# Kernel optimization log

Measured on AMD Instinct MI355X. Metric: run time of the kernel, lower is better.

Reference implementation:

```python
import jax, jax.numpy as jnp
import numpy as np

N_NODES = 100000
N_EDGES = 1600000
N_GRAPHS = 1024
F_NODE = 16
F_EDGE = 8
F_GRAPH = 10
F_OUT = 1
H = 64
EPS = 1e-7  # GENConv eps
T = 1.0     # GENConv softmax temperature (learn_t=False default)


def _lin_init(key, fi, fo):
    kw, kb = jax.random.split(key)
    s = 1.0 / np.sqrt(fi)
    W = jax.random.uniform(kw, (fi, fo), jnp.float32, -s, s)
    b = jax.random.uniform(kb, (fo,), jnp.float32, -s, s)
    return W, b


def setup_inputs() -> dict:
    key = jax.random.key(0)
    ks = jax.random.split(key, 24)
    inp = {
        'x': jax.random.normal(ks[0], (N_NODES, F_NODE), jnp.float32),
        'edge_attr': jax.random.normal(ks[1], (N_EDGES, F_EDGE), jnp.float32),
        'graph_attr': jax.random.normal(ks[2], (N_GRAPHS, F_GRAPH), jnp.float32),
        'edge_index': jax.random.randint(ks[3], (2, N_EDGES), 0, N_NODES),
        'batch': jnp.sort(jax.random.randint(ks[4], (N_NODES,), 0, N_GRAPHS)),
    }
    inp['node_W'], inp['node_b'] = _lin_init(ks[5], F_NODE, H)
    inp['edge_W'], inp['edge_b'] = _lin_init(ks[6], F_EDGE, H)
    # three GENConv MLPs: Linear(H,2H) -> BN(identity @eval) -> ReLU -> Linear(2H,H)
    for i, k1, k2 in ((1, ks[7], ks[8]), (2, ks[9], ks[10]), (3, ks[11], ks[12])):
        inp[f'c{i}_W1'], inp[f'c{i}_b1'] = _lin_init(k1, H, 2 * H)
        inp[f'c{i}_W2'], inp[f'c{i}_b2'] = _lin_init(k2, 2 * H, H)
    inp['d1_W'], inp['d1_b'] = _lin_init(ks[13], H + F_GRAPH, 32)
    inp['d2_W'], inp['d2_b'] = _lin_init(ks[14], 32, 32)
    inp['out_W'], inp['out_b'] = _lin_init(ks[15], 32, F_OUT)
    return inp


def _genconv(h, src, dst, ea, W1, b1, W2, b2):
    # message: relu(x_j + edge_attr) + eps   [E, H]
    msg = jax.nn.relu(h[src] + ea) + EPS
    # per-destination, per-feature segment softmax (aggr='softmax', t=1)
    m = jax.ops.segment_max(msg * T, dst, num_segments=N_NODES)   # [N, H]
    e = jnp.exp(msg * T - m[dst])                                  # [E, H]
    denom = jax.ops.segment_sum(e, dst, num_segments=N_NODES)     # [N, H]
    alpha = e / jnp.maximum(denom[dst], 1e-16)
    agg = jax.ops.segment_sum(msg * alpha, dst, num_segments=N_NODES)
    out = h + agg  # root add
    # MLP (BatchNorm is identity in eval with default stats)
    hid = jax.nn.relu(out @ W1 + b1)
    return hid @ W2 + b2


def reference(x, edge_attr, graph_attr, node_W, node_b, edge_W, edge_b,
              c1_W1, c1_b1, c1_W2, c1_b2,
              c2_W1, c2_b1, c2_W2, c2_b2,
              c3_W1, c3_b1, c3_W2, c3_b2,
              d1_W, d1_b, d2_W, d2_b, out_W, out_b,
              edge_index, batch):
    src, dst = edge_index[0], edge_index[1]
    h = x @ node_W + node_b
    ea = edge_attr @ edge_W + edge_b
    h = jax.nn.relu(_genconv(h, src, dst, ea, c1_W1, c1_b1, c1_W2, c1_b2))
    h = jax.nn.relu(_genconv(h, src, dst, ea, c2_W1, c2_b1, c2_W2, c2_b2))
    h = jax.nn.relu(_genconv(h, src, dst, ea, c3_W1, c3_b1, c3_W2, c3_b2))
    # global mean pool over graphs
    sums = jax.ops.segment_sum(h, batch, num_segments=N_GRAPHS)          # [G, H]
    cnt = jax.ops.segment_sum(jnp.ones((h.shape[0],), h.dtype), batch, num_segments=N_GRAPHS)
    pooled = sums / jnp.maximum(cnt, 1.0)[:, None]
    g = jnp.concatenate([pooled, graph_attr], axis=1)                    # [G, H+F_GRAPH]
    g = jax.nn.relu(g @ d1_W + d1_b)   # dropout = identity at eval
    g = jax.nn.relu(g @ d2_W + d2_b)
    return jax.nn.sigmoid(g @ out_W + out_b)                             # [G, 1]
```

## Files before the change

kernel.cpp:

```cpp
#include <hip/hip_runtime.h>
#include <hip/hip_bf16.h>

#define N_NODES 100000
#define N_EDGES 1600000
#define N_GRAPHS 1024
#define F_NODE 16
#define F_EDGE 8
#define F_GRAPH 10
#define HD 64
#define HD2 128
#define GEN_EPS 1e-7f
#define SCAN_NBLK ((N_NODES + 255) / 256)

typedef unsigned short u16;
typedef unsigned int u32;
typedef __attribute__((ext_vector_type(8))) short short8;
typedef __attribute__((ext_vector_type(4))) float floatx4;

__device__ __forceinline__ u16 f2bf(float x) {
    u32 u = __float_as_uint(x);
    return (u16)((u + 0x7FFFu + ((u >> 16) & 1u)) >> 16);
}
__device__ __forceinline__ float bf2f(u16 u) {
    return __uint_as_float(((u32)u) << 16);
}
__device__ __forceinline__ float u2f(unsigned int u) {
    return __uint_as_float(u);
}

__global__ void __launch_bounds__(256) k_node_embed(
        const float* __restrict__ x, const float* __restrict__ W,
        const float* __restrict__ b, float* __restrict__ h,
        u16* __restrict__ hb) {
    __shared__ float sW[F_NODE * HD];
    __shared__ float sb[HD];
    for (int i = threadIdx.x; i < F_NODE * HD; i += 256) sW[i] = W[i];
    if (threadIdx.x < HD) sb[threadIdx.x] = b[threadIdx.x];
    __syncthreads();
    int t = blockIdx.x * 256 + threadIdx.x;
    if (t >= N_NODES * HD) return;
    int n = t >> 6, f = t & 63;
    const float* xr = x + (size_t)n * F_NODE;
    float acc = sb[f];
#pragma unroll
    for (int k = 0; k < F_NODE; k++) acc += xr[k] * sW[k * HD + f];
    h[t] = acc;
    hb[t] = f2bf(acc);
}

__global__ void __launch_bounds__(256) k_hist(
        const int* __restrict__ dst, int* __restrict__ deg,
        int* __restrict__ rank) {
    int e = blockIdx.x * 256 + threadIdx.x;
    if (e >= N_EDGES) return;
    rank[e] = atomicAdd(&deg[dst[e]], 1);
}

__global__ void __launch_bounds__(256) k_scan1(
        const int* __restrict__ deg, int* __restrict__ bsum) {
    __shared__ int red[256];
    int t = threadIdx.x;
    int g = blockIdx.x * 256 + t;
    red[t] = (g < N_NODES) ? deg[g] : 0;
    __syncthreads();
    for (int s = 128; s > 0; s >>= 1) {
        if (t < s) red[t] += red[t + s];
        __syncthreads();
    }
    if (t == 0) bsum[blockIdx.x] = red[0];
}

__global__ void __launch_bounds__(512) k_scan2(
        const int* __restrict__ bsum, int* __restrict__ bpre) {
    __shared__ int sh[512];
    int t = threadIdx.x;
    int v = (t < SCAN_NBLK) ? bsum[t] : 0;
    sh[t] = v;
    __syncthreads();
    for (int d = 1; d < 512; d <<= 1) {
        int u = (t >= d) ? sh[t - d] : 0;
        __syncthreads();
        sh[t] += u;
        __syncthreads();
    }
    if (t < SCAN_NBLK) bpre[t] = sh[t] - v;
}

__global__ void __launch_bounds__(256) k_scan3(
        const int* __restrict__ deg, const int* __restrict__ bpre,
        int* __restrict__ off) {
    __shared__ int sh[256];
    int t = threadIdx.x;
    int g = blockIdx.x * 256 + t;
    int v = (g < N_NODES) ? deg[g] : 0;
    sh[t] = v;
    __syncthreads();
    for (int d = 1; d < 256; d <<= 1) {
        int u = (t >= d) ? sh[t - d] : 0;
        __syncthreads();
        sh[t] += u;
        __syncthreads();
    }
    int incl = sh[t];
    int base = bpre[blockIdx.x];
    if (g < N_NODES) off[g] = base + incl - v;
    if (g == N_NODES - 1) off[N_NODES] = base + incl;
}

__global__ void __launch_bounds__(256) k_scatter(
        const int* __restrict__ src, const int* __restrict__ dst,
        const int* __restrict__ rank, const int* __restrict__ off,
        const float* __restrict__ eattr,
        unsigned int* __restrict__ rec, int* __restrict__ srcs) {
    int e = blockIdx.x * 256 + threadIdx.x;
    if (e >= N_EDGES) return;
    const uint4* ap = reinterpret_cast<const uint4*>(eattr + (size_t)e * F_EDGE);
    uint4 a0 = ap[0], a1 = ap[1];
    int pos = off[dst[e]] + rank[e];
    uint4* op = reinterpret_cast<uint4*>(rec + (size_t)pos * 8);
    op[0] = a0;
    op[1] = a1;
    srcs[pos] = src[e];
}

__global__ void __launch_bounds__(256) k_gen_agg(
        const float* __restrict__ h, const u16* __restrict__ hb,
        const int* __restrict__ off,
        const unsigned int* __restrict__ rec,
        const int* __restrict__ srcs,
        const float* __restrict__ eW, const float* __restrict__ eb,
        float* __restrict__ outb) {
    __shared__ float sAttr[4][64];
    int wid = threadIdx.x >> 6;
    int lane = threadIdx.x & 63;
    int f = lane;
    float w[F_EDGE];
#pragma unroll
    for (int k = 0; k < F_EDGE; k++) w[k] = eW[k * HD + f];
    float bf = eb[f];
    int wave0 = blockIdx.x * 4 + wid;
    const int NW = gridDim.x * 4;
    for (int n0 = wave0; n0 < N_NODES; n0 += NW) {
        int n = __builtin_amdgcn_readfirstlane(n0);
        int beg = off[n], end = off[n + 1];
        size_t idx = (size_t)n * HD + f;
        float hroot = h[idx];
        float den = 0.f, nm = 0.f;
        if (beg < end) {
            int i = beg;
            float av = 0.f;
            if (beg + (lane >> 3) < end) av = u2f(rec[(size_t)beg * 8 + lane]);
            int s8[8];
#pragma unroll
            for (int u = 0; u < 8; u++) s8[u] = srcs[beg + u];
            while (true) {
                float hv[8];
#pragma unroll
                for (int u = 0; u < 8; u++)
                    hv[u] = bf2f(hb[(size_t)s8[u] * HD + f]);
                int inx = i + 8;
                bool more = inx < end;
                float avN = 0.f;
                int s8N[8];
                if (more) {
                    if (inx + (lane >> 3) < end)
                        avN = u2f(rec[(size_t)inx * 8 + lane]);
#pragma unroll
                    for (int u = 0; u < 8; u++) s8N[u] = srcs[inx + u];
                } else {
#pragma unroll
                    for (int u = 0; u < 8; u++) s8N[u] = 0;
                }
                sAttr[wid][lane] = av;
#pragma unroll
                for (int u = 0; u < 8; u++) {
                    if (i + u < end) {
                        const floatx4* A = reinterpret_cast<const floatx4*>(
                            &sAttr[wid][u * 8]);
                        floatx4 a0 = A[0], a1 = A[1];
                        float ea = bf + a0.x * w[0] + a0.y * w[1]
                                      + a0.z * w[2] + a0.w * w[3]
                                      + a1.x * w[4] + a1.y * w[5]
                                      + a1.z * w[6] + a1.w * w[7];
                        float r = fmaxf(hv[u] + ea, 0.f);
                        float ev = __expf(r);
                        den += ev;
                        nm += r * ev;
                    }
                }
                if (!more) break;
                i = inx;
                av = avN;
#pragma unroll
                for (int u = 0; u < 8; u++) s8[u] = s8N[u];
            }
        }
        float agg = (end > beg) ? (nm / fmaxf(den, 1e-16f) + GEN_EPS) : 0.f;
        outb[idx] = hroot + agg;
    }
}

__global__ void __launch_bounds__(256) k_mlp(
        const float* __restrict__ inb,
        const float* __restrict__ W1, const float* __restrict__ b1,
        const float* __restrict__ W2, const float* __restrict__ b2,
        float* __restrict__ hout, u16* __restrict__ hbout) {
    __shared__ u16 wB1[HD2][HD + 8];
    __shared__ u16 wB2[HD][HD2 + 8];
    __shared__ u16 sHid[64][HD2 + 8];
    __shared__ float sb1[HD2];
    __shared__ float sb2[HD];
    int tid = threadIdx.x;
    for (int i = tid; i < HD * HD2; i += 256) {
        int ff = i >> 7, j = i & 127;
        wB1[j][ff] = f2bf(W1[i]);
    }
    for (int i = tid; i < HD2 * HD; i += 256) {
        int j = i >> 6, c = i & 63;
        wB2[c][j] = f2bf(W2[i]);
    }
    if (tid < HD2) sb1[tid] = b1[tid];
    if (tid < HD) sb2[tid] = b2[tid];
    __syncthreads();
    int wid = tid >> 6, lane = tid & 63;
    int quad = lane >> 4, lm = lane & 15;
    int n0 = blockIdx.x * 64 + wid * 16;
    bool active = (n0 < N_NODES);
    if (active) {
        int node = n0 + lm;
        short8 a[2];
        const float* ar = inb + (size_t)node * HD;
#pragma unroll
        for (int kk = 0; kk < 2; kk++) {
            const float4* p = reinterpret_cast<const float4*>(ar + kk * 32 + quad * 8);
            float4 v0 = p[0], v1 = p[1];
            short8 t;
            t[0] = (short)f2bf(v0.x); t[1] = (short)f2bf(v0.y);
            t[2] = (short)f2bf(v0.z); t[3] = (short)f2bf(v0.w);
            t[4] = (short)f2bf(v1.x); t[5] = (short)f2bf(v1.y);
            t[6] = (short)f2bf(v1.z); t[7] = (short)f2bf(v1.w);
            a[kk] = t;
        }
#pragma unroll
        for (int jt = 0; jt < 8; jt++) {
            int jb = jt * 16;
            float bias = sb1[jb + lm];
            floatx4 acc = {bias, bias, bias, bias};
#pragma unroll
            for (int kk = 0; kk < 2; kk++) {
                const short8* bp = reinterpret_cast<const short8*>(
                    &wB1[jb + lm][kk * 32 + quad * 8]);
                acc = __builtin_amdgcn_mfma_f32_16x16x32_bf16(a[kk], *bp, acc, 0, 0, 0);
            }
#pragma unroll
            for (int r = 0; r < 4; r++) {
                int lr = wid * 16 + quad * 4 + r;
                sHid[lr][jb + lm] = f2bf(fmaxf(acc[r], 0.f));
            }
        }
    }
    __syncthreads();
    if (active) {
        short8 a2[4];
#pragma unroll
        for (int kk = 0; kk < 4; kk++)
            a2[kk] = *reinterpret_cast<const short8*>(
                &sHid[wid * 16 + lm][kk * 32 + quad * 8]);
#pragma unroll
        for (int ct = 0; ct < 4; ct++) {
            int cb = ct * 16;
            float bias = sb2[cb + lm];
            floatx4 acc = {bias, bias, bias, bias};
#pragma unroll
            for (int kk = 0; kk < 4; kk++) {
                const short8* bp = reinterpret_cast<const short8*>(
                    &wB2[cb + lm][kk * 32 + quad * 8]);
                acc = __builtin_amdgcn_mfma_f32_16x16x32_bf16(a2[kk], *bp, acc, 0, 0, 0);
            }
#pragma unroll
            for (int r = 0; r < 4; r++) {
                int orow = n0 + quad * 4 + r;
                float o = fmaxf(acc[r], 0.f);
                hout[(size_t)orow * HD + cb + lm] = o;
                hbout[(size_t)orow * HD + cb + lm] = f2bf(o);
            }
        }
    }
}

__global__ void __launch_bounds__(256) k_pool(
        const float* __restrict__ h, const int* __restrict__ batch,
        float* __restrict__ pooled) {
    int g = blockIdx.x * 4 + (threadIdx.x >> 6);
    if (g >= N_GRAPHS) return;
    int f = threadIdx.x & 63;
    int lo = 0, hi = N_NODES;
    while (lo < hi) {
        int mid = (lo + hi) >> 1;
        if (batch[mid] < g) lo = mid + 1; else hi = mid;
    }
    int b = lo;
    int lo2 = b, hi2 = N_NODES;
    while (lo2 < hi2) {
        int mid = (lo2 + hi2) >> 1;
        if (batch[mid] < g + 1) lo2 = mid + 1; else hi2 = mid;
    }
    int e = lo2;
    float s = 0.f;
    for (int n = b; n < e; n++) s += h[(size_t)n * HD + f];
    float cnt = fmaxf((float)(e - b), 1.f);
    pooled[(size_t)g * HD + f] = s / cnt;
}

__global__ void __launch_bounds__(64) k_head(
        const float* __restrict__ pooled, const float* __restrict__ gattr,
        const float* __restrict__ d1W, const float* __restrict__ d1b,
        const float* __restrict__ d2W, const float* __restrict__ d2b,
        const float* __restrict__ oW, const float* __restrict__ ob,
        float* __restrict__ out) {
    int g = blockIdx.x;
    __shared__ float si[HD + F_GRAPH];
    __shared__ float s1[32], s2[32];
    int t = threadIdx.x;
    if (t < HD) si[t] = pooled[(size_t)g * HD + t];
    if (t < F_GRAPH) si[HD + t] = gattr[(size_t)g * F_GRAPH + t];
    __syncthreads();
    if (t < 32) {
        float acc = d1b[t];
        for (int i = 0; i < HD + F_GRAPH; i++) acc += si[i] * d1W[i * 32 + t];
        s1[t] = fmaxf(acc, 0.f);
    }
    __syncthreads();
    if (t < 32) {
        float acc = d2b[t];
        for (int i = 0; i < 32; i++) acc += s1[i] * d2W[i * 32 + t];
        s2[t] = fmaxf(acc, 0.f);
    }
    __syncthreads();
    if (t == 0) {
        float acc = ob[0];
        for (int i = 0; i < 32; i++) acc += s2[i] * oW[i];
        out[g] = 1.f / (1.f + __expf(-acc));
    }
}

extern "C" void kernel_launch(void* const* d_in, const int* in_sizes, int n_in,
                              void* d_out, int out_size, void* d_ws, size_t ws_size,
                              hipStream_t stream) {
    const float* x     = (const float*)d_in[0];
    const float* eattr = (const float*)d_in[1];
    const float* gattr = (const float*)d_in[2];
    const int*   eidx  = (const int*)d_in[3];
    const int*   batch = (const int*)d_in[4];
    const float* nodeW = (const float*)d_in[5];
    const float* nodeb = (const float*)d_in[6];
    const float* edgeW = (const float*)d_in[7];
    const float* edgeb = (const float*)d_in[8];
    const float* cW1[3] = {(const float*)d_in[9],  (const float*)d_in[13], (const float*)d_in[17]};
    const float* cb1[3] = {(const float*)d_in[10], (const float*)d_in[14], (const float*)d_in[18]};
    const float* cW2[3] = {(const float*)d_in[11], (const float*)d_in[15], (const float*)d_in[19]};
    const float* cb2[3] = {(const float*)d_in[12], (const float*)d_in[16], (const float*)d_in[20]};
    const float* d1W = (const float*)d_in[21];
    const float* d1b = (const float*)d_in[22];
    const float* d2W = (const float*)d_in[23];
    const float* d2b = (const float*)d_in[24];
    const float* oW  = (const float*)d_in[25];
    const float* ob  = (const float*)d_in[26];

    const int* src = eidx;
    const int* dst = eidx + N_EDGES;

    char* p = (char*)d_ws;
    float* h      = (float*)p; p += (size_t)N_NODES * HD * 4;
    float* outb   = (float*)p; p += (size_t)N_NODES * HD * 4;
    int*   srcs   = (int*)p;   p += (size_t)(N_EDGES + 64) * 4;
    unsigned int* rec = (unsigned int*)p; p += (size_t)(N_EDGES + 8) * F_EDGE * 4;
    u16*   hb     = (u16*)p;   p += (size_t)N_NODES * HD * 2;
    float* pooled = (float*)p; p += (size_t)N_GRAPHS * HD * 4;
    int*   off    = (int*)p;   p += (size_t)(N_NODES + 1) * 4;
    int*   deg    = (int*)p;   p += (size_t)N_NODES * 4;
    int*   rank   = (int*)p;   p += (size_t)N_EDGES * 4;
    int*   bsum   = (int*)p;   p += (size_t)(SCAN_NBLK + 1) * 4;
    int*   bpre   = (int*)p;   p += (size_t)(SCAN_NBLK + 1) * 4;

    const int EB = (N_EDGES + 255) / 256;
    const int NBM = (N_NODES + 63) / 64;

    k_node_embed<<<(N_NODES * HD + 255) / 256, 256, 0, stream>>>(x, nodeW, nodeb, h, hb);

    hipMemsetAsync(deg, 0, (size_t)N_NODES * 4, stream);
    hipMemsetAsync(srcs + N_EDGES, 0, 64 * sizeof(int), stream);
    k_hist<<<EB, 256, 0, stream>>>(dst, deg, rank);
    k_scan1<<<SCAN_NBLK, 256, 0, stream>>>(deg, bsum);
    k_scan2<<<1, 512, 0, stream>>>(bsum, bpre);
    k_scan3<<<SCAN_NBLK, 256, 0, stream>>>(deg, bpre, off);
    k_scatter<<<EB, 256, 0, stream>>>(src, dst, rank, off, eattr, rec, srcs);

    for (int l = 0; l < 3; l++) {
        k_gen_agg<<<2048, 256, 0, stream>>>(
            h, hb, off, rec, srcs, edgeW, edgeb, outb);
        k_mlp<<<NBM, 256, 0, stream>>>(outb, cW1[l], cb1[l], cW2[l], cb2[l], h, hb);
    }

    k_pool<<<(N_GRAPHS + 3) / 4, 256, 0, stream>>>(h, batch, pooled);
    k_head<<<N_GRAPHS, 64, 0, stream>>>(pooled, gattr,
                                        d1W, d1b, d2W, d2b, oW, ob,
                                        (float*)d_out);
}
```

Measured before the change: 698.9 us.

## Fuse GENConv aggregation and MLP into one per-layer kernel with pre-transposed weights

Merges the softmax aggregation kernel and the MLP kernel into a single per-layer kernel. Each wave aggregates 16 nodes into shared memory and then runs the two MFMA layers on them directly, so the fp32 intermediate buffer no longer makes a round trip through global memory. The bf16 weight transposes move into a one-time prep kernel, and the MLP reads them from global memory instead of staging them in LDS per block. Node features are ping-ponged between two buffers to avoid read/write hazards. The cost is that each wave walks 16 nodes serially with no grid-stride balancing, and weight reads now depend on cache hits.

```diff
diff --git a/kernel.cpp b/kernel.cpp
--- a/kernel.cpp
+++ b/kernel.cpp
@@ -123,117 +123,117 @@
     srcs[pos] = src[e];
 }
 
-__global__ void __launch_bounds__(256) k_gen_agg(
-        const float* __restrict__ h, const u16* __restrict__ hb,
+__global__ void __launch_bounds__(256) k_prep(
+        const float* __restrict__ W1a, const float* __restrict__ W2a,
+        const float* __restrict__ W1b, const float* __restrict__ W2b,
+        const float* __restrict__ W1c, const float* __restrict__ W2c,
+        u16* __restrict__ W1t, u16* __restrict__ W2t) {
+    int bid = blockIdx.x;
+    int l = bid >> 6;
+    int t = (bid & 63) * 256 + threadIdx.x;
+    const float* W1 = (l == 0) ? W1a : (l == 1) ? W1b : W1c;
+    const float* W2 = (l == 0) ? W2a : (l == 1) ? W2b : W2c;
+    if (t < HD * HD2) {
+        int j = t >> 6, k = t & 63;
+        W1t[(size_t)l * HD * HD2 + t] = f2bf(W1[k * HD2 + j]);
+    } else {
+        int u = t - HD * HD2;
+        int c = u >> 7, j = u & 127;
+        W2t[(size_t)l * HD * HD2 + u] = f2bf(W2[j * HD + c]);
+    }
+}
+
+__global__ void __launch_bounds__(256, 8) k_layer(
+        const float* __restrict__ hin, const u16* __restrict__ hbin,
         const int* __restrict__ off,
         const unsigned int* __restrict__ rec,
         const int* __restrict__ srcs,
         const float* __restrict__ eW, const float* __restrict__ eb,
-        float* __restrict__ outb) {
+        const u16* __restrict__ W1t, const float* __restrict__ b1,
+        const u16* __restrict__ W2t, const float* __restrict__ b2,
+        float* __restrict__ hout, u16* __restrict__ hbout) {
+    __shared__ float segf[4][16 * 73 + 4];
     __shared__ float sAttr[4][64];
     int wid = threadIdx.x >> 6;
     int lane = threadIdx.x & 63;
-    int f = lane;
-    float w[F_EDGE];
-#pragma unroll
-    for (int k = 0; k < F_EDGE; k++) w[k] = eW[k * HD + f];
-    float bf = eb[f];
-    int wave0 = blockIdx.x * 4 + wid;
-    const int NW = gridDim.x * 4;
-    for (int n0 = wave0; n0 < N_NODES; n0 += NW) {
-        int n = __builtin_amdgcn_readfirstlane(n0);
-        int beg = off[n], end = off[n + 1];
-        size_t idx = (size_t)n * HD + f;
-        float hroot = h[idx];
-        float den = 0.f, nm = 0.f;
-        if (beg < end) {
-            int i = beg;
-            float av = 0.f;
-            if (beg + (lane >> 3) < end) av = u2f(rec[(size_t)beg * 8 + lane]);
-            int s8[8];
-#pragma unroll
-            for (int u = 0; u < 8; u++) s8[u] = srcs[beg + u];
-            while (true) {
-                float hv[8];
-#pragma unroll
-                for (int u = 0; u < 8; u++)
-                    hv[u] = bf2f(hb[(size_t)s8[u] * HD + f]);
-                int inx = i + 8;
-                bool more = inx < end;
-                float avN = 0.f;
-                int s8N[8];
-                if (more) {
-                    if (inx + (lane >> 3) < end)
-                        avN = u2f(rec[(size_t)inx * 8 + lane]);
-#pragma unroll
-                    for (int u = 0; u < 8; u++) s8N[u] = srcs[inx + u];
-                } else {
-#pragma unroll
-                    for (int u = 0; u < 8; u++) s8N[u] = 0;
+    float* sAggW = segf[wid];
+    u16* sHidW = (u16*)segf[wid];
+    int nt0 = blockIdx.x * 64 + wid * 16;
+    if (nt0 >= N_NODES) return;
+
+    {
+        int f = lane;
+        float w[F_EDGE];
+#pragma unroll
+        for (int k = 0; k < F_EDGE; k++) w[k] = eW[k * HD + f];
+        float bfv = eb[f];
+        for (int j = 0; j < 16; j++) {
+            int n = nt0 + j;
+            int beg = off[n], end = off[n + 1];
+            float hroot = hin[(size_t)n * HD + f];
+            float den = 0.f, nm = 0.f;
+            if (beg < end) {
+                int i = beg;
+                float av = 0.f;
+                if (beg + (lane >> 3) < end) av = u2f(rec[(size_t)beg * 8 + lane]);
+                int s8[8];
+#pragma unroll
+                for (int u = 0; u < 8; u++) s8[u] = srcs[beg + u];
+                while (true) {
+                    float hv[8];
+#pragma unroll
+                    for (int u = 0; u < 8; u++)
+                        hv[u] = bf2f(hbin[(size_t)s8[u] * HD + f]);
+                    int inx = i + 8;
+                    bool more = inx < end;
+                    float avN = 0.f;
+                    int s8N[8];
+                    if (more) {
+                        if (inx + (lane >> 3) < end)
+                            avN = u2f(rec[(size_t)inx * 8 + lane]);
+#pragma unroll
+                        for (int u = 0; u < 8; u++) s8N[u] = srcs[inx + u];
+                    } else {
+#pragma unroll
+                        for (int u = 0; u < 8; u++) s8N[u] = 0;
+                    }
+                    sAttr[wid][lane] = av;
+#pragma unroll
+                    for (int u = 0; u < 8; u++) {
+                        if (i + u < end) {
+                            const floatx4* A = reinterpret_cast<const floatx4*>(
+                                &sAttr[wid][u * 8]);
+                            floatx4 a0 = A[0], a1 = A[1];
+                            float ea = bfv + a0.x * w[0] + a0.y * w[1]
+                                           + a0.z * w[2] + a0.w * w[3]
+                                           + a1.x * w[4] + a1.y * w[5]
+                                           + a1.z * w[6] + a1.w * w[7];
+                            float r = fmaxf(hv[u] + ea, 0.f);
+                            float ev = __expf(r);
+                            den += ev;
+                            nm += r * ev;
+                        }
+                    }
+                    if (!more) break;
+                    i = inx;
+                    av = avN;
+#pragma unroll
+                    for (int u = 0; u < 8; u++) s8[u] = s8N[u];
                 }
-                sAttr[wid][lane] = av;
-#pragma unroll
-                for (int u = 0; u < 8; u++) {
-                    if (i + u < end) {
-                        const floatx4* A = reinterpret_cast<const floatx4*>(
-                            &sAttr[wid][u * 8]);
-                        floatx4 a0 = A[0], a1 = A[1];
-                        float ea = bf + a0.x * w[0] + a0.y * w[1]
-                                      + a0.z * w[2] + a0.w * w[3]
-                                      + a1.x * w[4] + a1.y * w[5]
-                                      + a1.z * w[6] + a1.w * w[7];
-                        float r = fmaxf(hv[u] + ea, 0.f);
-                        float ev = __expf(r);
-                        den += ev;
-                        nm += r * ev;
-                    }
-                }
-                if (!more) break;
-                i = inx;
-                av = avN;
-#pragma unroll
-                for (int u = 0; u < 8; u++) s8[u] = s8N[u];
             }
+            float agg = (end > beg) ? (nm / fmaxf(den, 1e-16f) + GEN_EPS) : 0.f;
+            sAggW[j * 73 + f] = hroot + agg;
         }
-        float agg = (end > beg) ? (nm / fmaxf(den, 1e-16f) + GEN_EPS) : 0.f;
-        outb[idx] = hroot + agg;
-    }
-}
-
-__global__ void __launch_bounds__(256) k_mlp(
-        const float* __restrict__ inb,
-        const float* __restrict__ W1, const float* __restrict__ b1,
-        const float* __restrict__ W2, const float* __restrict__ b2,
-        float* __restrict__ hout, u16* __restrict__ hbout) {
-    __shared__ u16 wB1[HD2][HD + 8];
-    __shared__ u16 wB2[HD][HD2 + 8];
-    __shared__ u16 sHid[64][HD2 + 8];
-    __shared__ float sb1[HD2];
-    __shared__ float sb2[HD];
-    int tid = threadIdx.x;
-    for (int i = tid; i < HD * HD2; i += 256) {
-        int ff = i >> 7, j = i & 127;
-        wB1[j][ff] = f2bf(W1[i]);
-    }
-    for (int i = tid; i < HD2 * HD; i += 256) {
-        int j = i >> 6, c = i & 63;
-        wB2[c][j] = f2bf(W2[i]);
-    }
-    if (tid < HD2) sb1[tid] = b1[tid];
-    if (tid < HD) sb2[tid] = b2[tid];
-    __syncthreads();
-    int wid = tid >> 6, lane = tid & 63;
-    int quad = lane >> 4, lm = lane & 15;
-    int n0 = blockIdx.x * 64 + wid * 16;
-    bool active = (n0 < N_NODES);
-    if (active) {
-        int node = n0 + lm;
+    }
+
+    {
+        int quad = lane >> 4, lm = lane & 15;
         short8 a[2];
-        const float* ar = inb + (size_t)node * HD;
 #pragma unroll
         for (int kk = 0; kk < 2; kk++) {
-            const float4* p = reinterpret_cast<const float4*>(ar + kk * 32 + quad * 8);
-            float4 v0 = p[0], v1 = p[1];
+            const floatx4* p = reinterpret_cast<const floatx4*>(
+                &sAggW[lm * 73 + kk * 32 + quad * 8]);
+            floatx4 v0 = p[0], v1 = p[1];
             short8 t;
             t[0] = (short)f2bf(v0.x); t[1] = (short)f2bf(v0.y);
             t[2] = (short)f2bf(v0.z); t[3] = (short)f2bf(v0.w);
@@ -244,42 +244,37 @@
 #pragma unroll
         for (int jt = 0; jt < 8; jt++) {
             int jb = jt * 16;
-            float bias = sb1[jb + lm];
+            float bias = b1[jb + lm];
             floatx4 acc = {bias, bias, bias, bias};
 #pragma unroll
             for (int kk = 0; kk < 2; kk++) {
                 const short8* bp = reinterpret_cast<const short8*>(
-                    &wB1[jb + lm][kk * 32 + quad * 8]);
+                    W1t + (size_t)(jb + lm) * HD + kk * 32 + quad * 8);
                 acc = __builtin_amdgcn_mfma_f32_16x16x32_bf16(a[kk], *bp, acc, 0, 0, 0);
             }
 #pragma unroll
-            for (int r = 0; r < 4; r++) {
-                int lr = wid * 16 + quad * 4 + r;
-                sHid[lr][jb + lm] = f2bf(fmaxf(acc[r], 0.f));
-            }
+            for (int r = 0; r < 4; r++)
+                sHidW[(quad * 4 + r) * 136 + jb + lm] = f2bf(fmaxf(acc[r], 0.f));
         }
-    }
-    __syncthreads();
-    if (active) {
         short8 a2[4];
 #pragma unroll
         for (int kk = 0; kk < 4; kk++)
             a2[kk] = *reinterpret_cast<const short8*>(
-                &sHid[wid * 16 + lm][kk * 32 + quad * 8]);
+                &sHidW[lm * 136 + kk * 32 + quad * 8]);
 #pragma unroll
         for (int ct = 0; ct < 4; ct++) {
             int cb = ct * 16;
-            float bias = sb2[cb + lm];
+            float bias = b2[cb + lm];
             floatx4 acc = {bias, bias, bias, bias};
 #pragma unroll
             for (int kk = 0; kk < 4; kk++) {
                 const short8* bp = reinterpret_cast<const short8*>(
-                    &wB2[cb + lm][kk * 32 + quad * 8]);
+                    W2t + (size_t)(cb + lm) * HD2 + kk * 32 + quad * 8);
                 acc = __builtin_amdgcn_mfma_f32_16x16x32_bf16(a2[kk], *bp, acc, 0, 0, 0);
             }
 #pragma unroll
             for (int r = 0; r < 4; r++) {
-                int orow = n0 + quad * 4 + r;
+                int orow = nt0 + quad * 4 + r;
                 float o = fmaxf(acc[r], 0.f);
                 hout[(size_t)orow * HD + cb + lm] = o;
                 hbout[(size_t)orow * HD + cb + lm] = f2bf(o);
@@ -372,10 +367,13 @@
 
     char* p = (char*)d_ws;
     float* h      = (float*)p; p += (size_t)N_NODES * HD * 4;
-    float* outb   = (float*)p; p += (size_t)N_NODES * HD * 4;
+    float* h2     = (float*)p; p += (size_t)N_NODES * HD * 4;
     int*   srcs   = (int*)p;   p += (size_t)(N_EDGES + 64) * 4;
     unsigned int* rec = (unsigned int*)p; p += (size_t)(N_EDGES + 8) * F_EDGE * 4;
     u16*   hb     = (u16*)p;   p += (size_t)N_NODES * HD * 2;
+    u16*   hb2    = (u16*)p;   p += (size_t)N_NODES * HD * 2;
+    u16*   W1t    = (u16*)p;   p += (size_t)3 * HD * HD2 * 2;
+    u16*   W2t    = (u16*)p;   p += (size_t)3 * HD * HD2 * 2;
     float* pooled = (float*)p; p += (size_t)N_GRAPHS * HD * 4;
     int*   off    = (int*)p;   p += (size_t)(N_NODES + 1) * 4;
     int*   deg    = (int*)p;   p += (size_t)N_NODES * 4;
@@ -384,9 +382,11 @@
     int*   bpre   = (int*)p;   p += (size_t)(SCAN_NBLK + 1) * 4;
 
     const int EB = (N_EDGES + 255) / 256;
-    const int NBM = (N_NODES + 63) / 64;
+    const int NBL = (N_NODES + 63) / 64;
 
     k_node_embed<<<(N_NODES * HD + 255) / 256, 256, 0, stream>>>(x, nodeW, nodeb, h, hb);
+    k_prep<<<192, 256, 0, stream>>>(cW1[0], cW2[0], cW1[1], cW2[1], cW1[2], cW2[2],
+                                    W1t, W2t);
 
     hipMemsetAsync(deg, 0, (size_t)N_NODES * 4, stream);
     hipMemsetAsync(srcs + N_EDGES, 0, 64 * sizeof(int), stream);
@@ -396,13 +396,19 @@
     k_scan3<<<SCAN_NBLK, 256, 0, stream>>>(deg, bpre, off);
     k_scatter<<<EB, 256, 0, stream>>>(src, dst, rank, off, eattr, rec, srcs);
 
+    float* ha = h;  u16* hba = hb;
+    float* hc = h2; u16* hbc = hb2;
     for (int l = 0; l < 3; l++) {
-        k_gen_agg<<<2048, 256, 0, stream>>>(
-            h, hb, off, rec, srcs, edgeW, edgeb, outb);
-        k_mlp<<<NBM, 256, 0, stream>>>(outb, cW1[l], cb1[l], cW2[l], cb2[l], h, hb);
-    }
-
-    k_pool<<<(N_GRAPHS + 3) / 4, 256, 0, stream>>>(h, batch, pooled);
+        k_layer<<<NBL, 256, 0, stream>>>(
+            ha, hba, off, rec, srcs, edgeW, edgeb,
+            W1t + (size_t)l * HD * HD2, cb1[l],
+            W2t + (size_t)l * HD * HD2, cb2[l],
+            hc, hbc);
+        float* tf = ha; ha = hc; hc = tf;
+        u16* tu = hba; hba = hbc; hbc = tu;
+    }
+
+    k_pool<<<(N_GRAPHS + 3) / 4, 256, 0, stream>>>(ha, batch, pooled);
     k_head<<<N_GRAPHS, 64, 0, stream>>>(pooled, gattr,
                                         d1W, d1b, d2W, d2b, oW, ob,
                                         (float*)d_out);
```

Measured after the change: 738.1 us. +5.6%, slower.

## Pre-convert MLP weights once and unroll edge aggregation by sixteen

Applied to the files above, without the earlier changes.

Adds a prep kernel that converts and transposes all three layers' MLP weights to bf16 in global memory once. k_mlp then reads those weight fragments straight from global/L2 and no longer rebuilds them in LDS in every block, which also removes the block-wide sync. Separately, the edge aggregation loop now processes 16 neighbours per iteration with 16 outstanding gathers, to expose more memory-level parallelism. In exchange, nodes with low degree waste more predicated work per iteration, register pressure rises, and MLP weight reads now go through the cache instead of LDS.

```diff
diff --git a/kernel.cpp b/kernel.cpp
--- a/kernel.cpp
+++ b/kernel.cpp
@@ -123,6 +123,26 @@
     srcs[pos] = src[e];
 }
 
+__global__ void __launch_bounds__(256) k_prep(
+        const float* __restrict__ W1a, const float* __restrict__ W2a,
+        const float* __restrict__ W1b, const float* __restrict__ W2b,
+        const float* __restrict__ W1c, const float* __restrict__ W2c,
+        u16* __restrict__ W1t, u16* __restrict__ W2t) {
+    int bid = blockIdx.x;
+    int l = bid >> 6;
+    int t = (bid & 63) * 256 + threadIdx.x;
+    const float* W1 = (l == 0) ? W1a : (l == 1) ? W1b : W1c;
+    const float* W2 = (l == 0) ? W2a : (l == 1) ? W2b : W2c;
+    if (t < HD * HD2) {
+        int j = t >> 6, k = t & 63;
+        W1t[(size_t)l * HD * HD2 + t] = f2bf(W1[k * HD2 + j]);
+    } else {
+        int u = t - HD * HD2;
+        int c = u >> 7, j = u & 127;
+        W2t[(size_t)l * HD * HD2 + u] = f2bf(W2[j * HD + c]);
+    }
+}
+
 __global__ void __launch_bounds__(256) k_gen_agg(
         const float* __restrict__ h, const u16* __restrict__ hb,
         const int* __restrict__ off,
@@ -130,14 +150,14 @@
         const int* __restrict__ srcs,
         const float* __restrict__ eW, const float* __restrict__ eb,
         float* __restrict__ outb) {
-    __shared__ float sAttr[4][64];
+    __shared__ float sAttr[4][128];
     int wid = threadIdx.x >> 6;
     int lane = threadIdx.x & 63;
     int f = lane;
     float w[F_EDGE];
 #pragma unroll
     for (int k = 0; k < F_EDGE; k++) w[k] = eW[k * HD + f];
-    float bf = eb[f];
+    float bfv = eb[f];
     int wave0 = blockIdx.x * 4 + wid;
     const int NW = gridDim.x * 4;
     for (int n0 = wave0; n0 < N_NODES; n0 += NW) {
@@ -148,40 +168,45 @@
         float den = 0.f, nm = 0.f;
         if (beg < end) {
             int i = beg;
-            float av = 0.f;
-            if (beg + (lane >> 3) < end) av = u2f(rec[(size_t)beg * 8 + lane]);
-            int s8[8];
-#pragma unroll
-            for (int u = 0; u < 8; u++) s8[u] = srcs[beg + u];
+            float av0 = 0.f, av1 = 0.f;
+            if (beg + (lane >> 3) < end) av0 = u2f(rec[(size_t)beg * 8 + lane]);
+            if (beg + 8 + (lane >> 3) < end)
+                av1 = u2f(rec[(size_t)(beg + 8) * 8 + lane]);
+            int s16[16];
+#pragma unroll
+            for (int u = 0; u < 16; u++) s16[u] = srcs[beg + u];
             while (true) {
-                float hv[8];
-#pragma unroll
-                for (int u = 0; u < 8; u++)
-                    hv[u] = bf2f(hb[(size_t)s8[u] * HD + f]);
-                int inx = i + 8;
+                float hv[16];
+#pragma unroll
+                for (int u = 0; u < 16; u++)
+                    hv[u] = bf2f(hb[(size_t)s16[u] * HD + f]);
+                int inx = i + 16;
                 bool more = inx < end;
-                float avN = 0.f;
-                int s8N[8];
+                float av0N = 0.f, av1N = 0.f;
+                int s16N[16];
                 if (more) {
                     if (inx + (lane >> 3) < end)
-                        avN = u2f(rec[(size_t)inx * 8 + lane]);
-#pragma unroll
-                    for (int u = 0; u < 8; u++) s8N[u] = srcs[inx + u];
+                        av0N = u2f(rec[(size_t)inx * 8 + lane]);
+                    if (inx + 8 + (lane >> 3) < end)
+                        av1N = u2f(rec[(size_t)(inx + 8) * 8 + lane]);
+#pragma unroll
+                    for (int u = 0; u < 16; u++) s16N[u] = srcs[inx + u];
                 } else {
 #pragma unroll
-                    for (int u = 0; u < 8; u++) s8N[u] = 0;
+                    for (int u = 0; u < 16; u++) s16N[u] = 0;
                 }
-                sAttr[wid][lane] = av;
-#pragma unroll
-                for (int u = 0; u < 8; u++) {
+                sAttr[wid][lane] = av0;
+                sAttr[wid][64 + lane] = av1;
+#pragma unroll
+                for (int u = 0; u < 16; u++) {
                     if (i + u < end) {
                         const floatx4* A = reinterpret_cast<const floatx4*>(
                             &sAttr[wid][u * 8]);
                         floatx4 a0 = A[0], a1 = A[1];
-                        float ea = bf + a0.x * w[0] + a0.y * w[1]
-                                      + a0.z * w[2] + a0.w * w[3]
-                                      + a1.x * w[4] + a1.y * w[5]
-                                      + a1.z * w[6] + a1.w * w[7];
+                        float ea = bfv + a0.x * w[0] + a0.y * w[1]
+                                       + a0.z * w[2] + a0.w * w[3]
+                                       + a1.x * w[4] + a1.y * w[5]
+                                       + a1.z * w[6] + a1.w * w[7];
                         float r = fmaxf(hv[u] + ea, 0.f);
                         float ev = __expf(r);
                         den += ev;
@@ -190,9 +215,10 @@
                 }
                 if (!more) break;
                 i = inx;
-                av = avN;
-#pragma unroll
-                for (int u = 0; u < 8; u++) s8[u] = s8N[u];
+                av0 = av0N;
+                av1 = av1N;
+#pragma unroll
+                for (int u = 0; u < 16; u++) s16[u] = s16N[u];
             }
         }
         float agg = (end > beg) ? (nm / fmaxf(den, 1e-16f) + GEN_EPS) : 0.f;
@@ -202,88 +228,68 @@
 
 __global__ void __launch_bounds__(256) k_mlp(
         const float* __restrict__ inb,
-        const float* __restrict__ W1, const float* __restrict__ b1,
-        const float* __restrict__ W2, const float* __restrict__ b2,
+        const u16* __restrict__ W1t, const float* __restrict__ b1,
+        const u16* __restrict__ W2t, const float* __restrict__ b2,
         float* __restrict__ hout, u16* __restrict__ hbout) {
-    __shared__ u16 wB1[HD2][HD + 8];
-    __shared__ u16 wB2[HD][HD2 + 8];
     __shared__ u16 sHid[64][HD2 + 8];
-    __shared__ float sb1[HD2];
-    __shared__ float sb2[HD];
     int tid = threadIdx.x;
-    for (int i = tid; i < HD * HD2; i += 256) {
-        int ff = i >> 7, j = i & 127;
-        wB1[j][ff] = f2bf(W1[i]);
-    }
-    for (int i = tid; i < HD2 * HD; i += 256) {
-        int j = i >> 6, c = i & 63;
-        wB2[c][j] = f2bf(W2[i]);
-    }
-    if (tid < HD2) sb1[tid] = b1[tid];
-    if (tid < HD) sb2[tid] = b2[tid];
-    __syncthreads();
     int wid = tid >> 6, lane = tid & 63;
     int quad = lane >> 4, lm = lane & 15;
     int n0 = blockIdx.x * 64 + wid * 16;
-    bool active = (n0 < N_NODES);
-    if (active) {
-        int node = n0 + lm;
-        short8 a[2];
-        const float* ar = inb + (size_t)node * HD;
+    if (n0 >= N_NODES) return;
+    int node = n0 + lm;
+    short8 a[2];
+    const float* ar = inb + (size_t)node * HD;
+#pragma unroll
+    for (int kk = 0; kk < 2; kk++) {
+        const float4* p = reinterpret_cast<const float4*>(ar + kk * 32 + quad * 8);
+        float4 v0 = p[0], v1 = p[1];
+        short8 t;
+        t[0] = (short)f2bf(v0.x); t[1] = (short)f2bf(v0.y);
+        t[2] = (short)f2bf(v0.z); t[3] = (short)f2bf(v0.w);
+        t[4] = (short)f2bf(v1.x); t[5] = (short)f2bf(v1.y);
+        t[6] = (short)f2bf(v1.z); t[7] = (short)f2bf(v1.w);
+        a[kk] = t;
+    }
+#pragma unroll
+    for (int jt = 0; jt < 8; jt++) {
+        int jb = jt * 16;
+        float bias = b1[jb + lm];
+        floatx4 acc = {bias, bias, bias, bias};
 #pragma unroll
         for (int kk = 0; kk < 2; kk++) {
-            const float4* p = reinterpret_cast<const float4*>(ar + kk * 32 + quad * 8);
-            float4 v0 = p[0], v1 = p[1];
-            short8 t;
-            t[0] = (short)f2bf(v0.x); t[1] = (short)f2bf(v0.y);
-            t[2] = (short)f2bf(v0.z); t[3] = (short)f2bf(v0.w);
-            t[4] = (short)f2bf(v1.x); t[5] = (short)f2bf(v1.y);
-            t[6] = (short)f2bf(v1.z); t[7] = (short)f2bf(v1.w);
-            a[kk] = t;
+            const short8* bp = reinterpret_cast<const short8*>(
+                W1t + (size_t)(jb + lm) * HD + kk * 32 + quad * 8);
+            acc = __builtin_amdgcn_mfma_f32_16x16x32_bf16(a[kk], *bp, acc, 0, 0, 0);
         }
 #pragma unroll
-        for (int jt = 0; jt < 8; jt++) {
-            int jb = jt * 16;
-            float bias = sb1[jb + lm];
-            floatx4 acc = {bias, bias, bias, bias};
-#pragma unroll
-            for (int kk = 0; kk < 2; kk++) {
-                const short8* bp = reinterpret_cast<const short8*>(
-                    &wB1[jb + lm][kk * 32 + quad * 8]);
-                acc = __builtin_amdgcn_mfma_f32_16x16x32_bf16(a[kk], *bp, acc, 0, 0, 0);
-            }
-#pragma unroll
-            for (int r = 0; r < 4; r++) {
-                int lr = wid * 16 + quad * 4 + r;
-                sHid[lr][jb + lm] = f2bf(fmaxf(acc[r], 0.f));
-            }
+        for (int r = 0; r < 4; r++) {
+            int lr = wid * 16 + quad * 4 + r;
+            sHid[lr][jb + lm] = f2bf(fmaxf(acc[r], 0.f));
         }
     }
-    __syncthreads();
-    if (active) {
-        short8 a2[4];
-#pragma unroll
-        for (int kk = 0; kk < 4; kk++)
-            a2[kk] = *reinterpret_cast<const short8*>(
-                &sHid[wid * 16 + lm][kk * 32 + quad * 8]);
-#pragma unroll
-        for (int ct = 0; ct < 4; ct++) {
-            int cb = ct * 16;
-            float bias = sb2[cb + lm];
-            floatx4 acc = {bias, bias, bias, bias};
-#pragma unroll
-            for (int kk = 0; kk < 4; kk++) {
-                const short8* bp = reinterpret_cast<const short8*>(
-                    &wB2[cb + lm][kk * 32 + quad * 8]);
-                acc = __builtin_amdgcn_mfma_f32_16x16x32_bf16(a2[kk], *bp, acc, 0, 0, 0);
-            }
-#pragma unroll
-            for (int r = 0; r < 4; r++) {
-                int orow = n0 + quad * 4 + r;
-                float o = fmaxf(acc[r], 0.f);
-                hout[(size_t)orow * HD + cb + lm] = o;
-                hbout[(size_t)orow * HD + cb + lm] = f2bf(o);
-            }
+    short8 a2[4];
+#pragma unroll
+    for (int kk = 0; kk < 4; kk++)
+        a2[kk] = *reinterpret_cast<const short8*>(
+            &sHid[wid * 16 + lm][kk * 32 + quad * 8]);
+#pragma unroll
+    for (int ct = 0; ct < 4; ct++) {
+        int cb = ct * 16;
+        float bias = b2[cb + lm];
+        floatx4 acc = {bias, bias, bias, bias};
+#pragma unroll
+        for (int kk = 0; kk < 4; kk++) {
+            const short8* bp = reinterpret_cast<const short8*>(
+                W2t + (size_t)(cb + lm) * HD2 + kk * 32 + quad * 8);
+            acc = __builtin_amdgcn_mfma_f32_16x16x32_bf16(a2[kk], *bp, acc, 0, 0, 0);
+        }
+#pragma unroll
+        for (int r = 0; r < 4; r++) {
+            int orow = n0 + quad * 4 + r;
+            float o = fmaxf(acc[r], 0.f);
+            hout[(size_t)orow * HD + cb + lm] = o;
+            hbout[(size_t)orow * HD + cb + lm] = f2bf(o);
         }
     }
 }
@@ -376,6 +382,8 @@
     int*   srcs   = (int*)p;   p += (size_t)(N_EDGES + 64) * 4;
     unsigned int* rec = (unsigned int*)p; p += (size_t)(N_EDGES + 8) * F_EDGE * 4;
     u16*   hb     = (u16*)p;   p += (size_t)N_NODES * HD * 2;
+    u16*   W1t    = (u16*)p;   p += (size_t)3 * HD * HD2 * 2;
+    u16*   W2t    = (u16*)p;   p += (size_t)3 * HD * HD2 * 2;
     float* pooled = (float*)p; p += (size_t)N_GRAPHS * HD * 4;
     int*   off    = (int*)p;   p += (size_t)(N_NODES + 1) * 4;
     int*   deg    = (int*)p;   p += (size_t)N_NODES * 4;
@@ -387,6 +395,8 @@
     const int NBM = (N_NODES + 63) / 64;
 
     k_node_embed<<<(N_NODES * HD + 255) / 256, 256, 0, stream>>>(x, nodeW, nodeb, h, hb);
+    k_prep<<<192, 256, 0, stream>>>(cW1[0], cW2[0], cW1[1], cW2[1], cW1[2], cW2[2],
+                                    W1t, W2t);
 
     hipMemsetAsync(deg, 0, (size_t)N_NODES * 4, stream);
     hipMemsetAsync(srcs + N_EDGES, 0, 64 * sizeof(int), stream);
@@ -399,7 +409,10 @@
     for (int l = 0; l < 3; l++) {
         k_gen_agg<<<2048, 256, 0, stream>>>(
             h, hb, off, rec, srcs, edgeW, edgeb, outb);
-        k_mlp<<<NBM, 256, 0, stream>>>(outb, cW1[l], cb1[l], cW2[l], cb2[l], h, hb);
+        k_mlp<<<NBM, 256, 0, stream>>>(outb,
+                                       W1t + (size_t)l * HD * HD2, cb1[l],
+                                       W2t + (size_t)l * HD * HD2, cb2[l],
+                                       h, hb);
     }
 
     k_pool<<<(N_GRAPHS + 3) / 4, 256, 0, stream>>>(h, batch, pooled);
```

Result: no change. 712.6 us (+2.0%).
